# Kernel optimization log

Hardware: AMD Instinct MI355X
Metric: run time of the kernel (lower is better)

## Reference

```python
import jax, jax.numpy as jnp
import numpy as np

N_NODES = 100000


def setup_inputs() -> dict:
    key = jax.random.key(0)
    k1, k2, k3 = jax.random.split(key, 3)
    feat = jax.random.normal(k1, (N_NODES, 64), dtype=jnp.float32)
    src = jax.random.randint(k2, (1250000,), 0, N_NODES, dtype=jnp.int64)
    dst = jax.random.randint(k3, (1250000,), 0, N_NODES, dtype=jnp.int64)
    return {"feat": feat, "src": src, "dst": dst}


def reference(feat, src, dst):
    # GraphConv(norm='both', activation=None): degree-normalized neighbor sum
    # with implicit self-connection (rst = feat_dst + sum_neighbors), where
    # degrees are clamp(min=1) + 1 to account for the self edge.
    n = feat.shape[0]
    ones = jnp.ones(src.shape[0], dtype=feat.dtype)
    out_deg = jax.ops.segment_sum(ones, src, num_segments=n)
    in_deg = jax.ops.segment_sum(ones, dst, num_segments=n)
    norm_l = jax.lax.rsqrt(jnp.maximum(out_deg, 1.0) + 1.0)  # [N]
    norm_r = jax.lax.rsqrt(jnp.maximum(in_deg, 1.0) + 1.0)   # [N]
    feat_src = feat * norm_l[:, None]                         # left-normalize
    msgs = feat_src[src]                                      # gather [E, D]
    h_neigh = jax.ops.segment_sum(msgs, dst, num_segments=n)  # scatter-sum [N, D]
    rst = (feat + h_neigh) * norm_r[:, None]                  # right-normalize
    return rst
```

## Files before the change

### kernel.cpp

```cpp
#include <hip/hip_runtime.h>


#define GC_D 64
#define GC_CAP 64
#define PBITS 8
#define PSIZE 256
#define SCAP 4096
#define EPB 8192
#define MAXPART 512


__global__ void zero_int_kernel(int* __restrict__ p, int n) {
    int i = blockIdx.x * blockDim.x + threadIdx.x;
    if (i < n) p[i] = 0;
}

__global__ __launch_bounds__(512) void partition_kernel(
        const int* __restrict__ src,
        const int* __restrict__ dst,
        int* __restrict__ curA,
        int* __restrict__ curB,
        int* __restrict__ streamA,
        unsigned char* __restrict__ streamB,
        int e, int nPart) {
    __shared__ int histA[MAXPART], histB[MAXPART], baseA[MAXPART], baseB[MAXPART];
    __shared__ int lcurA[MAXPART], lcurB[MAXPART];
    int t = threadIdx.x;
    for (int i = t; i < nPart; i += 512) {
        histA[i] = 0; histB[i] = 0; lcurA[i] = 0; lcurB[i] = 0;
    }
    __syncthreads();
    int lo = blockIdx.x * EPB;
    int hi = min(lo + EPB, e);
    for (int i = lo + t; i < hi; i += 512) {
        int s = src[i], d = dst[i];
        atomicAdd(&histA[d >> PBITS], 1);
        atomicAdd(&histB[s >> PBITS], 1);
    }
    __syncthreads();
    for (int i = t; i < nPart; i += 512) {
        int hA = histA[i];
        baseA[i] = hA ? atomicAdd(&curA[i], hA) : 0;
        int hB = histB[i];
        baseB[i] = hB ? atomicAdd(&curB[i], hB) : 0;
    }
    __syncthreads();
    for (int i = lo + t; i < hi; i += 512) {
        int s = src[i], d = dst[i];
        int pA = d >> PBITS;
        int posA = baseA[pA] + atomicAdd(&lcurA[pA], 1);
        if (posA < SCAP) streamA[pA * SCAP + posA] = s | ((d & 255) << 17);
        int pB = s >> PBITS;
        int posB = baseB[pB] + atomicAdd(&lcurB[pB], 1);
        if (posB < SCAP) streamB[pB * SCAP + posB] = (unsigned char)(s & 255);
    }
}

__global__ __launch_bounds__(512) void build_kernel(
        const int* __restrict__ curA,
        const int* __restrict__ curB,
        const int* __restrict__ streamA,
        const unsigned char* __restrict__ streamB,
        const float* __restrict__ feat,
        int* __restrict__ cnt,
        unsigned short* __restrict__ featb,
        int* __restrict__ bucket,
        int n) {
    __shared__ int lcur[PSIZE], lodeg[PSIZE];
    __shared__ int lbucket[PSIZE * GC_CAP];
    int p = blockIdx.x, t = threadIdx.x;
    if (t < PSIZE) { lcur[t] = 0; lodeg[t] = 0; }
    __syncthreads();
    int cA = min(curA[p], SCAP);
    int cB = min(curB[p], SCAP);
    const int* sA = streamA + (size_t)p * SCAP;
    const unsigned char* sB = streamB + (size_t)p * SCAP;
    for (int i = t; i < cA; i += 512) {
        int entry = sA[i];
        int bin = (entry >> 17) & 255;
        int pos = atomicAdd(&lcur[bin], 1);
        if (pos < GC_CAP) lbucket[bin * GC_CAP + pos] = entry & 0x1FFFF;
    }
    for (int i = t; i < cB; i += 512) atomicAdd(&lodeg[sB[i]], 1);
    __syncthreads();
    int g = p * PSIZE;
    if (t < PSIZE && g + t < n) cnt[g + t] = lcur[t];
    int4* dstw = (int4*)(bucket + (size_t)p * PSIZE * GC_CAP);
    const int4* srcw = (const int4*)lbucket;
#pragma unroll
    for (int i = 0; i < (PSIZE * GC_CAP / 4) / 512; ++i)
        dstw[i * 512 + t] = srcw[i * 512 + t];
    int wave = t >> 6, lane = t & 63;
    for (int r = wave; r < PSIZE; r += 8) {
        int node = g + r;
        if (node >= n) break;
        float nl = rsqrtf(fmaxf((float)lodeg[r], 1.0f) + 1.0f);
        float v = feat[(size_t)node * GC_D + lane] * nl;
        unsigned bb = __float_as_uint(v);
        bb = (bb + 0x7FFFu + ((bb >> 16) & 1u)) >> 16;
        featb[(size_t)node * GC_D + lane] = (unsigned short)bb;
    }
    if (p == 0 && t < GC_D) featb[(size_t)n * GC_D + t] = 0;
}

__global__ __launch_bounds__(256) void gather_bf16_kernel(
        const float* __restrict__ feat,
        const unsigned short* __restrict__ featb,
        const int* __restrict__ bucket,
        const int* __restrict__ cnt,
        float* __restrict__ out,
        int n) {
    int wid = (blockIdx.x * blockDim.x + threadIdx.x) >> 6;
    int lane = threadIdx.x & 63;
    if (wid >= n) return;
    int deg = cnt[wid];
    int s_raw = bucket[wid * GC_CAP + lane];
    int m = min(deg, GC_CAP);
    int s_l = (lane < m) ? s_raw : n;
    int half = lane >> 5;
    int c = lane & 31;
    float acc0 = 0.0f, acc1 = 0.0f;
    int m16 = (m + 15) & ~15;
    for (int j = 0; j < m16; j += 16) {
#pragma unroll
        for (int k = 0; k < 8; ++k) {
            int s = __shfl(s_l, j + 2 * k + half);
            unsigned u = *(const unsigned*)(featb + (size_t)s * GC_D + 2 * c);
            acc0 += __uint_as_float(u << 16);
            acc1 += __uint_as_float(u & 0xFFFF0000u);
        }
    }
    acc0 += __shfl_xor(acc0, 32);
    acc1 += __shfl_xor(acc1, 32);
    if (half == 0) {
        float nr = rsqrtf(fmaxf((float)deg, 1.0f) + 1.0f);
        const float2 self = *(const float2*)(feat + (size_t)wid * GC_D + 2 * c);
        float2 r;
        r.x = (self.x + acc0) * nr;
        r.y = (self.y + acc1) * nr;
        *(float2*)(out + (size_t)wid * GC_D + 2 * c) = r;
    }
}


__global__ void bucket_hist_kernel(const int* __restrict__ src,
                                   const int* __restrict__ dst,
                                   int* __restrict__ cnt,
                                   int* __restrict__ outdeg,
                                   int* __restrict__ bucket,
                                   int e) {
    int i = blockIdx.x * blockDim.x + threadIdx.x;
    if (i < e) {
        int s = src[i];
        int d = dst[i];
        atomicAdd(&outdeg[s], 1);
        int pos = atomicAdd(&cnt[d], 1);
        if (pos < GC_CAP) bucket[d * GC_CAP + pos] = s;
    }
}

__global__ void convert_kernel(const float* __restrict__ feat,
                               const int* __restrict__ outdeg,
                               unsigned short* __restrict__ featb,
                               int n) {
    int i = blockIdx.x * blockDim.x + threadIdx.x;
    int total = (n + 1) * GC_D;
    if (i >= total) return;
    int row = i >> 6;
    if (row >= n) { featb[i] = 0; return; }
    float nl = rsqrtf(fmaxf((float)outdeg[row], 1.0f) + 1.0f);
    unsigned b = __float_as_uint(feat[i] * nl);
    b = (b + 0x7FFFu + ((b >> 16) & 1u)) >> 16;
    featb[i] = (unsigned short)b;
}


__global__ void hist_kernel(const int* __restrict__ src,
                            const int* __restrict__ dst,
                            int* __restrict__ outdeg,
                            int* __restrict__ indeg,
                            int e) {
    int i = blockIdx.x * blockDim.x + threadIdx.x;
    if (i < e) {
        atomicAdd(&outdeg[src[i]], 1);
        atomicAdd(&indeg[dst[i]], 1);
    }
}

__global__ void block_reduce_kernel(const int* __restrict__ indeg,
                                    int* __restrict__ partials,
                                    int n) {
    __shared__ int sdata[256];
    int t = threadIdx.x;
    int i = blockIdx.x * 256 + t;
    sdata[t] = (i < n) ? indeg[i] : 0;
    __syncthreads();
    for (int s = 128; s > 0; s >>= 1) {
        if (t < s) sdata[t] += sdata[t + s];
        __syncthreads();
    }
    if (t == 0) partials[blockIdx.x] = sdata[0];
}

__global__ void scan_partials_kernel(const int* __restrict__ partials,
                                     int* __restrict__ scanned,
                                     int P) {
    __shared__ int sdata[512];
    int t = threadIdx.x;
    int own = (t < P) ? partials[t] : 0;
    sdata[t] = own;
    __syncthreads();
    for (int off = 1; off < 512; off <<= 1) {
        int v = (t >= off) ? sdata[t - off] : 0;
        __syncthreads();
        sdata[t] += v;
        __syncthreads();
    }
    if (t < P) scanned[t] = sdata[t] - own;
}

__global__ void scan_final_kernel(const int* __restrict__ indeg,
                                  const int* __restrict__ outdeg,
                                  const int* __restrict__ scanned,
                                  int* __restrict__ offsets,
                                  int* __restrict__ cursors,
                                  float* __restrict__ norm_l,
                                  float* __restrict__ norm_r,
                                  int n) {
    __shared__ int sdata[256];
    int t = threadIdx.x;
    int i = blockIdx.x * 256 + t;
    int c = (i < n) ? indeg[i] : 0;
    sdata[t] = c;
    __syncthreads();
    for (int off = 1; off < 256; off <<= 1) {
        int v = (t >= off) ? sdata[t - off] : 0;
        __syncthreads();
        sdata[t] += v;
        __syncthreads();
    }
    if (i < n) {
        int excl = sdata[t] - c;
        int pos = scanned[blockIdx.x] + excl;
        offsets[i] = pos;
        cursors[i] = pos;
        norm_r[i] = rsqrtf(fmaxf((float)c, 1.0f) + 1.0f);
        norm_l[i] = rsqrtf(fmaxf((float)outdeg[i], 1.0f) + 1.0f);
    }
}

__global__ void bucket_kernel(const int* __restrict__ src,
                              const int* __restrict__ dst,
                              int* __restrict__ cursors,
                              int* __restrict__ perm_src,
                              int e) {
    int i = blockIdx.x * blockDim.x + threadIdx.x;
    if (i < e) {
        int d = dst[i];
        int pos = atomicAdd(&cursors[d], 1);
        perm_src[pos] = src[i];
    }
}

__global__ __launch_bounds__(256) void gather_csr_kernel(
        const float* __restrict__ feat,
        const int* __restrict__ perm_src,
        const int* __restrict__ offsets,
        const int* __restrict__ indeg,
        const float* __restrict__ norm_l,
        const float* __restrict__ norm_r,
        float* __restrict__ out,
        int n) {
    int wid = (blockIdx.x * blockDim.x + threadIdx.x) >> 6;
    int lane = threadIdx.x & 63;
    if (wid >= n) return;
    int off = offsets[wid];
    int deg = indeg[wid];
    float acc = 0.0f;
    for (int base = 0; base < deg; base += 64) {
        int m = min(64, deg - base);
        int s_l = 0;
        float nl_l = 0.0f;
        if (lane < m) {
            s_l = perm_src[off + base + lane];
            nl_l = norm_l[s_l];
        }
        for (int j = 0; j < m; ++j) {
            int s = __shfl(s_l, j);
            float nl = __shfl(nl_l, j);
            acc += feat[s * GC_D + lane] * nl;
        }
    }
    int oi = wid * GC_D + lane;
    out[oi] = (feat[oi] + acc) * norm_r[wid];
}


extern "C" void kernel_launch(void* const* d_in, const int* in_sizes, int n_in,
                              void* d_out, int out_size, void* d_ws, size_t ws_size,
                              hipStream_t stream) {
    const float* feat = (const float*)d_in[0];
    const int*   src  = (const int*)d_in[1];
    const int*   dst  = (const int*)d_in[2];
    float* out = (float*)d_out;

    const int n = in_sizes[0] / GC_D;
    const int e = in_sizes[1];
    const int P = (n + 255) / 256;
    const int nPart = (n + PSIZE - 1) >> PBITS;

    size_t bucket_ints = (size_t)nPart * PSIZE * GC_CAP;
    size_t featb_ints  = ((size_t)(n + 1) * GC_D + 1) / 2;
    size_t o = 2 * (size_t)nPart;
    o = (o + 3) & ~(size_t)3;
    size_t cnt_o = o;           o += n;
    o = (o + 31) & ~(size_t)31;
    size_t bucket_o = o;        o += bucket_ints;
    size_t featb_o = o;         o += featb_ints;
    size_t streamA_o = o;       o += (size_t)nPart * SCAP;
    size_t need_main = o * sizeof(int) + (size_t)nPart * SCAP;

    size_t featb_bytes = (size_t)(n + 1) * GC_D * sizeof(unsigned short);
    size_t need_bf16 = ((size_t)2 * n + (size_t)n * GC_CAP) * sizeof(int) + featb_bytes;
    size_t need_csr = ((size_t)6 * n + 2 * P + e) * sizeof(int);

    bool main_ok = (ws_size >= need_main) && nPart <= MAXPART && n <= 131071;

    if (main_ok) {
        int* ws = (int*)d_ws;
        int* curA   = ws;
        int* curB   = ws + nPart;
        int* cnt    = ws + cnt_o;
        int* bucket = ws + bucket_o;
        unsigned short* featb = (unsigned short*)(ws + featb_o);
        int* streamA = ws + streamA_o;
        unsigned char* streamB = (unsigned char*)(ws + o);

        zero_int_kernel<<<(2 * nPart + 255) / 256, 256, 0, stream>>>(curA, 2 * nPart);
        partition_kernel<<<(e + EPB - 1) / EPB, 512, 0, stream>>>(
            src, dst, curA, curB, streamA, streamB, e, nPart);
        build_kernel<<<nPart, 512, 0, stream>>>(curA, curB, streamA, streamB,
                                                feat, cnt, featb, bucket, n);
        long long total = (long long)n * GC_D;
        gather_bf16_kernel<<<(int)((total + 255) / 256), 256, 0, stream>>>(
            feat, featb, bucket, cnt, out, n);
    } else if (ws_size >= need_bf16) {
        int* cnt    = (int*)d_ws;
        int* outdeg = cnt + n;
        int* bucket = outdeg + n;
        unsigned short* featb = (unsigned short*)(bucket + (size_t)n * GC_CAP);

        zero_int_kernel<<<(2 * n + 255) / 256, 256, 0, stream>>>(cnt, 2 * n);
        bucket_hist_kernel<<<(e + 255) / 256, 256, 0, stream>>>(src, dst, cnt,
                                                                outdeg, bucket, e);
        int totalc = (n + 1) * GC_D;
        convert_kernel<<<(totalc + 255) / 256, 256, 0, stream>>>(feat, outdeg,
                                                                 featb, n);
        long long total = (long long)n * GC_D;
        gather_bf16_kernel<<<(int)((total + 255) / 256), 256, 0, stream>>>(
            feat, featb, bucket, cnt, out, n);
    } else if (ws_size >= need_csr && P <= 512) {
        int* indeg   = (int*)d_ws;
        int* outdeg  = indeg + n;
        int* offsets = outdeg + n;
        int* cursors = offsets + n;
        float* norm_l = (float*)(cursors + n);
        float* norm_r = norm_l + n;
        int* partials = (int*)(norm_r + n);
        int* scanned  = partials + P;
        int* perm_src = scanned + P;

        zero_int_kernel<<<(2 * n + 255) / 256, 256, 0, stream>>>(indeg, 2 * n);
        hist_kernel<<<(e + 255) / 256, 256, 0, stream>>>(src, dst, outdeg, indeg, e);
        block_reduce_kernel<<<P, 256, 0, stream>>>(indeg, partials, n);
        scan_partials_kernel<<<1, 512, 0, stream>>>(partials, scanned, P);
        scan_final_kernel<<<P, 256, 0, stream>>>(indeg, outdeg, scanned, offsets,
                                                 cursors, norm_l, norm_r, n);
        bucket_kernel<<<(e + 255) / 256, 256, 0, stream>>>(src, dst, cursors, perm_src, e);
        long long total = (long long)n * GC_D;
        gather_csr_kernel<<<(int)((total + 255) / 256), 256, 0, stream>>>(
            feat, perm_src, offsets, indeg, norm_l, norm_r, out, n);
    }
}
```

Before: 166.0 us.

## Fuse per-partition bucket sort into gather kernel, drop global bucket array

The build kernel no longer writes a padded per-node bucket array and count array to global memory. A new kernel loads each partition's edge stream into shared memory, does a local counting sort by destination, and gathers bf16 features for the partition's 256 nodes directly, with 16 waves per block. A separate kernel handles only out-degree and bf16 conversion. This removes the global bucket write and reread plus the 64-neighbor cap, but the gather now runs with one 1024-thread block per partition (about 391 blocks), which may limit parallelism. The zero kernel is replaced by a memset, and the unused CSR fallback is deleted.

```diff
diff --git a/kernel.cpp b/kernel.cpp
--- a/kernel.cpp
+++ b/kernel.cpp
@@ -2,18 +2,13 @@
 
 
 #define GC_D 64
-#define GC_CAP 64
 #define PBITS 8
 #define PSIZE 256
 #define SCAP 4096
 #define EPB 8192
 #define MAXPART 512
-
-
-__global__ void zero_int_kernel(int* __restrict__ p, int n) {
-    int i = blockIdx.x * blockDim.x + threadIdx.x;
-    if (i < n) p[i] = 0;
-}
+#define GC_CAP 64
+
 
 __global__ __launch_bounds__(512) void partition_kernel(
         const int* __restrict__ src,
@@ -56,41 +51,22 @@
     }
 }
 
-__global__ __launch_bounds__(512) void build_kernel(
-        const int* __restrict__ curA,
+__global__ __launch_bounds__(512) void convertB_kernel(
         const int* __restrict__ curB,
-        const int* __restrict__ streamA,
         const unsigned char* __restrict__ streamB,
         const float* __restrict__ feat,
-        int* __restrict__ cnt,
         unsigned short* __restrict__ featb,
-        int* __restrict__ bucket,
         int n) {
-    __shared__ int lcur[PSIZE], lodeg[PSIZE];
-    __shared__ int lbucket[PSIZE * GC_CAP];
+    __shared__ int lodeg[PSIZE];
     int p = blockIdx.x, t = threadIdx.x;
-    if (t < PSIZE) { lcur[t] = 0; lodeg[t] = 0; }
-    __syncthreads();
-    int cA = min(curA[p], SCAP);
+    if (t < PSIZE) lodeg[t] = 0;
+    __syncthreads();
     int cB = min(curB[p], SCAP);
-    const int* sA = streamA + (size_t)p * SCAP;
     const unsigned char* sB = streamB + (size_t)p * SCAP;
-    for (int i = t; i < cA; i += 512) {
-        int entry = sA[i];
-        int bin = (entry >> 17) & 255;
-        int pos = atomicAdd(&lcur[bin], 1);
-        if (pos < GC_CAP) lbucket[bin * GC_CAP + pos] = entry & 0x1FFFF;
-    }
     for (int i = t; i < cB; i += 512) atomicAdd(&lodeg[sB[i]], 1);
     __syncthreads();
+    int wave = t >> 6, lane = t & 63;
     int g = p * PSIZE;
-    if (t < PSIZE && g + t < n) cnt[g + t] = lcur[t];
-    int4* dstw = (int4*)(bucket + (size_t)p * PSIZE * GC_CAP);
-    const int4* srcw = (const int4*)lbucket;
-#pragma unroll
-    for (int i = 0; i < (PSIZE * GC_CAP / 4) / 512; ++i)
-        dstw[i * 512 + t] = srcw[i * 512 + t];
-    int wave = t >> 6, lane = t & 63;
     for (int r = wave; r < PSIZE; r += 8) {
         int node = g + r;
         if (node >= n) break;
@@ -101,6 +77,118 @@
         featb[(size_t)node * GC_D + lane] = (unsigned short)bb;
     }
     if (p == 0 && t < GC_D) featb[(size_t)n * GC_D + t] = 0;
+}
+
+__global__ __launch_bounds__(1024) void sortgather_kernel(
+        const int* __restrict__ curA,
+        const int* __restrict__ streamA,
+        const float* __restrict__ feat,
+        const unsigned short* __restrict__ featb,
+        float* __restrict__ out,
+        int n) {
+    __shared__ int sAl[SCAP];
+    __shared__ int lperm[SCAP];
+    __shared__ int lcnt[PSIZE], loff[PSIZE], lcur[PSIZE];
+    int p = blockIdx.x, t = threadIdx.x;
+    if (t < PSIZE) lcnt[t] = 0;
+    __syncthreads();
+    int cA = min(curA[p], SCAP);
+    const int* sA = streamA + (size_t)p * SCAP;
+    for (int i = t; i < cA; i += 1024) {
+        int v = sA[i];
+        sAl[i] = v;
+        atomicAdd(&lcnt[(v >> 17) & 255], 1);
+    }
+    __syncthreads();
+    if (t < PSIZE) loff[t] = lcnt[t];
+    __syncthreads();
+    for (int off = 1; off < PSIZE; off <<= 1) {
+        int a = (t < PSIZE && t >= off) ? loff[t - off] : 0;
+        __syncthreads();
+        if (t < PSIZE) loff[t] += a;
+        __syncthreads();
+    }
+    if (t < PSIZE) { loff[t] -= lcnt[t]; lcur[t] = 0; }
+    __syncthreads();
+    for (int i = t; i < cA; i += 1024) {
+        int v = sAl[i];
+        int bin = (v >> 17) & 255;
+        int pos = loff[bin] + atomicAdd(&lcur[bin], 1);
+        lperm[pos] = v & 0x1FFFF;
+    }
+    __syncthreads();
+    int wave = t >> 6, lane = t & 63;
+    int half = lane >> 5;
+    int c = lane & 31;
+    int g = p * PSIZE;
+    for (int r = wave; r < PSIZE; r += 16) {
+        int node = g + r;
+        if (node >= n) break;
+        int deg = lcnt[r];
+        int off = loff[r];
+        float acc0 = 0.0f, acc1 = 0.0f;
+        for (int base = 0; base < deg; base += 64) {
+            int m = min(deg - base, 64);
+            int s_l = (lane < m) ? lperm[off + base + lane] : n;
+            int m16 = (m + 15) & ~15;
+            for (int j = 0; j < m16; j += 16) {
+#pragma unroll
+                for (int k = 0; k < 8; ++k) {
+                    int s = __shfl(s_l, j + 2 * k + half);
+                    unsigned u = *(const unsigned*)(featb + (size_t)s * GC_D + 2 * c);
+                    acc0 += __uint_as_float(u << 16);
+                    acc1 += __uint_as_float(u & 0xFFFF0000u);
+                }
+            }
+        }
+        acc0 += __shfl_xor(acc0, 32);
+        acc1 += __shfl_xor(acc1, 32);
+        if (half == 0) {
+            float nr = rsqrtf(fmaxf((float)deg, 1.0f) + 1.0f);
+            const float2 self = *(const float2*)(feat + (size_t)node * GC_D + 2 * c);
+            float2 rr;
+            rr.x = (self.x + acc0) * nr;
+            rr.y = (self.y + acc1) * nr;
+            *(float2*)(out + (size_t)node * GC_D + 2 * c) = rr;
+        }
+    }
+}
+
+
+__global__ void zero_int_kernel(int* __restrict__ p, int n) {
+    int i = blockIdx.x * blockDim.x + threadIdx.x;
+    if (i < n) p[i] = 0;
+}
+
+__global__ void bucket_hist_kernel(const int* __restrict__ src,
+                                   const int* __restrict__ dst,
+                                   int* __restrict__ cnt,
+                                   int* __restrict__ outdeg,
+                                   int* __restrict__ bucket,
+                                   int e) {
+    int i = blockIdx.x * blockDim.x + threadIdx.x;
+    if (i < e) {
+        int s = src[i];
+        int d = dst[i];
+        atomicAdd(&outdeg[s], 1);
+        int pos = atomicAdd(&cnt[d], 1);
+        if (pos < GC_CAP) bucket[d * GC_CAP + pos] = s;
+    }
+}
+
+__global__ void convert_kernel(const float* __restrict__ feat,
+                               const int* __restrict__ outdeg,
+                               unsigned short* __restrict__ featb,
+                               int n) {
+    int i = blockIdx.x * blockDim.x + threadIdx.x;
+    int total = (n + 1) * GC_D;
+    if (i >= total) return;
+    int row = i >> 6;
+    if (row >= n) { featb[i] = 0; return; }
+    float nl = rsqrtf(fmaxf((float)outdeg[row], 1.0f) + 1.0f);
+    unsigned b = __float_as_uint(feat[i] * nl);
+    b = (b + 0x7FFFu + ((b >> 16) & 1u)) >> 16;
+    featb[i] = (unsigned short)b;
 }
 
 __global__ __launch_bounds__(256) void gather_bf16_kernel(
@@ -143,159 +231,6 @@
 }
 
 
-__global__ void bucket_hist_kernel(const int* __restrict__ src,
-                                   const int* __restrict__ dst,
-                                   int* __restrict__ cnt,
-                                   int* __restrict__ outdeg,
-                                   int* __restrict__ bucket,
-                                   int e) {
-    int i = blockIdx.x * blockDim.x + threadIdx.x;
-    if (i < e) {
-        int s = src[i];
-        int d = dst[i];
-        atomicAdd(&outdeg[s], 1);
-        int pos = atomicAdd(&cnt[d], 1);
-        if (pos < GC_CAP) bucket[d * GC_CAP + pos] = s;
-    }
-}
-
-__global__ void convert_kernel(const float* __restrict__ feat,
-                               const int* __restrict__ outdeg,
-                               unsigned short* __restrict__ featb,
-                               int n) {
-    int i = blockIdx.x * blockDim.x + threadIdx.x;
-    int total = (n + 1) * GC_D;
-    if (i >= total) return;
-    int row = i >> 6;
-    if (row >= n) { featb[i] = 0; return; }
-    float nl = rsqrtf(fmaxf((float)outdeg[row], 1.0f) + 1.0f);
-    unsigned b = __float_as_uint(feat[i] * nl);
-    b = (b + 0x7FFFu + ((b >> 16) & 1u)) >> 16;
-    featb[i] = (unsigned short)b;
-}
-
-
-__global__ void hist_kernel(const int* __restrict__ src,
-                            const int* __restrict__ dst,
-                            int* __restrict__ outdeg,
-                            int* __restrict__ indeg,
-                            int e) {
-    int i = blockIdx.x * blockDim.x + threadIdx.x;
-    if (i < e) {
-        atomicAdd(&outdeg[src[i]], 1);
-        atomicAdd(&indeg[dst[i]], 1);
-    }
-}
-
-__global__ void block_reduce_kernel(const int* __restrict__ indeg,
-                                    int* __restrict__ partials,
-                                    int n) {
-    __shared__ int sdata[256];
-    int t = threadIdx.x;
-    int i = blockIdx.x * 256 + t;
-    sdata[t] = (i < n) ? indeg[i] : 0;
-    __syncthreads();
-    for (int s = 128; s > 0; s >>= 1) {
-        if (t < s) sdata[t] += sdata[t + s];
-        __syncthreads();
-    }
-    if (t == 0) partials[blockIdx.x] = sdata[0];
-}
-
-__global__ void scan_partials_kernel(const int* __restrict__ partials,
-                                     int* __restrict__ scanned,
-                                     int P) {
-    __shared__ int sdata[512];
-    int t = threadIdx.x;
-    int own = (t < P) ? partials[t] : 0;
-    sdata[t] = own;
-    __syncthreads();
-    for (int off = 1; off < 512; off <<= 1) {
-        int v = (t >= off) ? sdata[t - off] : 0;
-        __syncthreads();
-        sdata[t] += v;
-        __syncthreads();
-    }
-    if (t < P) scanned[t] = sdata[t] - own;
-}
-
-__global__ void scan_final_kernel(const int* __restrict__ indeg,
-                                  const int* __restrict__ outdeg,
-                                  const int* __restrict__ scanned,
-                                  int* __restrict__ offsets,
-                                  int* __restrict__ cursors,
-                                  float* __restrict__ norm_l,
-                                  float* __restrict__ norm_r,
-                                  int n) {
-    __shared__ int sdata[256];
-    int t = threadIdx.x;
-    int i = blockIdx.x * 256 + t;
-    int c = (i < n) ? indeg[i] : 0;
-    sdata[t] = c;
-    __syncthreads();
-    for (int off = 1; off < 256; off <<= 1) {
-        int v = (t >= off) ? sdata[t - off] : 0;
-        __syncthreads();
-        sdata[t] += v;
-        __syncthreads();
-    }
-    if (i < n) {
-        int excl = sdata[t] - c;
-        int pos = scanned[blockIdx.x] + excl;
-        offsets[i] = pos;
-        cursors[i] = pos;
-        norm_r[i] = rsqrtf(fmaxf((float)c, 1.0f) + 1.0f);
-        norm_l[i] = rsqrtf(fmaxf((float)outdeg[i], 1.0f) + 1.0f);
-    }
-}
-
-__global__ void bucket_kernel(const int* __restrict__ src,
-                              const int* __restrict__ dst,
-                              int* __restrict__ cursors,
-                              int* __restrict__ perm_src,
-                              int e) {
-    int i = blockIdx.x * blockDim.x + threadIdx.x;
-    if (i < e) {
-        int d = dst[i];
-        int pos = atomicAdd(&cursors[d], 1);
-        perm_src[pos] = src[i];
-    }
-}
-
-__global__ __launch_bounds__(256) void gather_csr_kernel(
-        const float* __restrict__ feat,
-        const int* __restrict__ perm_src,
-        const int* __restrict__ offsets,
-        const int* __restrict__ indeg,
-        const float* __restrict__ norm_l,
-        const float* __restrict__ norm_r,
-        float* __restrict__ out,
-        int n) {
-    int wid = (blockIdx.x * blockDim.x + threadIdx.x) >> 6;
-    int lane = threadIdx.x & 63;
-    if (wid >= n) return;
-    int off = offsets[wid];
-    int deg = indeg[wid];
-    float acc = 0.0f;
-    for (int base = 0; base < deg; base += 64) {
-        int m = min(64, deg - base);
-        int s_l = 0;
-        float nl_l = 0.0f;
-        if (lane < m) {
-            s_l = perm_src[off + base + lane];
-            nl_l = norm_l[s_l];
-        }
-        for (int j = 0; j < m; ++j) {
-            int s = __shfl(s_l, j);
-            float nl = __shfl(nl_l, j);
-            acc += feat[s * GC_D + lane] * nl;
-        }
-    }
-    int oi = wid * GC_D + lane;
-    out[oi] = (feat[oi] + acc) * norm_r[wid];
-}
-
-
 extern "C" void kernel_launch(void* const* d_in, const int* in_sizes, int n_in,
                               void* d_out, int out_size, void* d_ws, size_t ws_size,
                               hipStream_t stream) {
@@ -306,44 +241,34 @@
 
     const int n = in_sizes[0] / GC_D;
     const int e = in_sizes[1];
-    const int P = (n + 255) / 256;
     const int nPart = (n + PSIZE - 1) >> PBITS;
 
-    size_t bucket_ints = (size_t)nPart * PSIZE * GC_CAP;
-    size_t featb_ints  = ((size_t)(n + 1) * GC_D + 1) / 2;
+    size_t featb_ints = ((size_t)(n + 1) * GC_D + 1) / 2;
     size_t o = 2 * (size_t)nPart;
-    o = (o + 3) & ~(size_t)3;
-    size_t cnt_o = o;           o += n;
     o = (o + 31) & ~(size_t)31;
-    size_t bucket_o = o;        o += bucket_ints;
-    size_t featb_o = o;         o += featb_ints;
-    size_t streamA_o = o;       o += (size_t)nPart * SCAP;
+    size_t streamA_o = o;  o += (size_t)nPart * SCAP;
+    size_t featb_o = o;    o += featb_ints;
     size_t need_main = o * sizeof(int) + (size_t)nPart * SCAP;
 
     size_t featb_bytes = (size_t)(n + 1) * GC_D * sizeof(unsigned short);
     size_t need_bf16 = ((size_t)2 * n + (size_t)n * GC_CAP) * sizeof(int) + featb_bytes;
-    size_t need_csr = ((size_t)6 * n + 2 * P + e) * sizeof(int);
 
     bool main_ok = (ws_size >= need_main) && nPart <= MAXPART && n <= 131071;
 
     if (main_ok) {
         int* ws = (int*)d_ws;
-        int* curA   = ws;
-        int* curB   = ws + nPart;
-        int* cnt    = ws + cnt_o;
-        int* bucket = ws + bucket_o;
+        int* curA = ws;
+        int* curB = ws + nPart;
+        int* streamA = ws + streamA_o;
         unsigned short* featb = (unsigned short*)(ws + featb_o);
-        int* streamA = ws + streamA_o;
         unsigned char* streamB = (unsigned char*)(ws + o);
 
-        zero_int_kernel<<<(2 * nPart + 255) / 256, 256, 0, stream>>>(curA, 2 * nPart);
+        hipMemsetAsync(curA, 0, 2 * (size_t)nPart * sizeof(int), stream);
         partition_kernel<<<(e + EPB - 1) / EPB, 512, 0, stream>>>(
             src, dst, curA, curB, streamA, streamB, e, nPart);
-        build_kernel<<<nPart, 512, 0, stream>>>(curA, curB, streamA, streamB,
-                                                feat, cnt, featb, bucket, n);
-        long long total = (long long)n * GC_D;
-        gather_bf16_kernel<<<(int)((total + 255) / 256), 256, 0, stream>>>(
-            feat, featb, bucket, cnt, out, n);
+        convertB_kernel<<<nPart, 512, 0, stream>>>(curB, streamB, feat, featb, n);
+        sortgather_kernel<<<nPart, 1024, 0, stream>>>(curA, streamA, feat, featb,
+                                                      out, n);
     } else if (ws_size >= need_bf16) {
         int* cnt    = (int*)d_ws;
         int* outdeg = cnt + n;
@@ -359,26 +284,5 @@
         long long total = (long long)n * GC_D;
         gather_bf16_kernel<<<(int)((total + 255) / 256), 256, 0, stream>>>(
             feat, featb, bucket, cnt, out, n);
-    } else if (ws_size >= need_csr && P <= 512) {
-        int* indeg   = (int*)d_ws;
-        int* outdeg  = indeg + n;
-        int* offsets = outdeg + n;
-        int* cursors = offsets + n;
-        float* norm_l = (float*)(cursors + n);
-        float* norm_r = norm_l + n;
-        int* partials = (int*)(norm_r + n);
-        int* scanned  = partials + P;
-        int* perm_src = scanned + P;
-
-        zero_int_kernel<<<(2 * n + 255) / 256, 256, 0, stream>>>(indeg, 2 * n);
-        hist_kernel<<<(e + 255) / 256, 256, 0, stream>>>(src, dst, outdeg, indeg, e);
-        block_reduce_kernel<<<P, 256, 0, stream>>>(indeg, partials, n);
-        scan_partials_kernel<<<1, 512, 0, stream>>>(partials, scanned, P);
-        scan_final_kernel<<<P, 256, 0, stream>>>(indeg, outdeg, scanned, offsets,
-                                                 cursors, norm_l, norm_r, n);
-        bucket_kernel<<<(e + 255) / 256, 256, 0, stream>>>(src, dst, cursors, perm_src, e);
-        long long total = (long long)n * GC_D;
-        gather_csr_kernel<<<(int)((total + 255) / 256), 256, 0, stream>>>(
-            feat, perm_src, offsets, indeg, norm_l, norm_r, out, n);
-    }
-}
+    }
+}
```

Measured after the change: 163.5 us. About the same (-1.5%).
